# Kernel optimization log

Hardware: AMD Instinct MI355X
Metric: run time of the kernel (lower is better)

The kernel has to match this reference:

```python
import jax, jax.numpy as jnp
import numpy as np

B, S, D = 2, 2048, 1024
H = 16
HD = D // H  # head_dim = 64


def _xavier(key, shape):
    fan_out, fan_in = shape
    bound = jnp.sqrt(6.0 / (fan_in + fan_out))
    return jax.random.uniform(key, shape, jnp.float32, -bound, bound)


def setup_inputs() -> dict:
    key = jax.random.key(0)
    kx, kqkv, ko = jax.random.split(key, 3)
    x = jax.random.normal(kx, (B, S, D), jnp.float32)
    # torch nn.Linear stores weight as [out, in]; we keep that layout and use x @ W.T
    W_qkv = _xavier(kqkv, (3 * D, D))
    b_qkv = jnp.zeros((3 * D,), jnp.float32)
    W_o = _xavier(ko, (D, D))
    b_o = jnp.zeros((D,), jnp.float32)
    return {"x": x, "W_qkv": W_qkv, "b_qkv": b_qkv, "W_o": W_o, "b_o": b_o}


def reference(x, W_qkv, b_qkv, W_o, b_o):
    b, s, d = x.shape
    h, hd = H, HD
    # qkv projection: [b, s, 3d]
    qkv = jnp.einsum("bsd,ed->bse", x, W_qkv) + b_qkv
    # [b, s, h, 3*hd] -> [b, h, s, 3*hd]
    qkv = qkv.reshape(b, s, h, 3 * hd).transpose(0, 2, 1, 3)
    q, k, v = jnp.split(qkv, 3, axis=-1)
    scale = 1.0 / jnp.sqrt(jnp.asarray(hd, x.dtype))
    logits = jnp.einsum("bhqd,bhkd->bhqk", q, k) * scale
    attn = jax.nn.softmax(logits, axis=-1)
    values = jnp.einsum("bhqk,bhkd->bhqd", attn, v)
    values = values.transpose(0, 2, 1, 3).reshape(b, s, d)
    return jnp.einsum("bsd,ed->bse", values, W_o) + b_o
```

## Files before the change

### kernel.cpp

```cpp
#include <hip/hip_runtime.h>

typedef unsigned short u16;
typedef __attribute__((ext_vector_type(8))) short bf16x8;
typedef __attribute__((ext_vector_type(4))) float f32x4;
typedef __attribute__((ext_vector_type(16))) float f32x16;
typedef __attribute__((ext_vector_type(4))) unsigned short u16x4;

__device__ __forceinline__ u16 f2bf(float f) {
    unsigned u = __float_as_uint(f);
    u = u + 0x7FFFu + ((u >> 16) & 1u);
    return (u16)(u >> 16);
}

__device__ __forceinline__ void gload16(const void* g, void* l) {
    __builtin_amdgcn_global_load_lds(
        (const __attribute__((address_space(1))) unsigned int*)g,
        (__attribute__((address_space(3))) unsigned int*)l,
        16, 0, 0);
}

__device__ __forceinline__ f32x4 mfma16(bf16x8 a, bf16x8 b, f32x4 c) {
    return __builtin_amdgcn_mfma_f32_16x16x32_bf16(a, b, c, 0, 0, 0);
}
__device__ __forceinline__ f32x16 mfma32(bf16x8 a, bf16x8 b, f32x16 c) {
    return __builtin_amdgcn_mfma_f32_32x32x16_bf16(a, b, c, 0, 0, 0);
}

__global__ __launch_bounds__(256) void cvt_all(const float* __restrict__ x,
                                               const float* __restrict__ wqkv,
                                               const float* __restrict__ wo,
                                               u16* __restrict__ dst) {
    int i = blockIdx.x * 256 + threadIdx.x;
    float4 v;
    if (i < 1048576)       v = ((const float4*)x)[i];
    else if (i < 1835008)  v = ((const float4*)wqkv)[i - 1048576];
    else                   v = ((const float4*)wo)[i - 1835008];
    u16x4 o = { f2bf(v.x), f2bf(v.y), f2bf(v.z), f2bf(v.w) };
    ((u16x4*)dst)[i] = o;
}

template <int BM, int BN, bool OUT_BF16>
__global__ __launch_bounds__(256) void gemm_bt(const u16* __restrict__ A,
                                               const u16* __restrict__ Bm,
                                               const float* __restrict__ bias,
                                               void* __restrict__ Cp,
                                               int M, int N, int K) {
    constexpr int FM = BM / 32, FN = BN / 32;
    __shared__ u16 As[2][BM * 64];
    __shared__ u16 Bs[2][BN * 64];
    const int tid = threadIdx.x, lane = tid & 63, wave = tid >> 6;
    const int wr = wave >> 1, wc = wave & 1;
    const int l15 = lane & 15, l4 = lane >> 4;

    const int nx = gridDim.x, nwg = nx * gridDim.y;
    const int id = blockIdx.y * nx + blockIdx.x;
    const int wg = (id & 7) * (nwg >> 3) + (id >> 3);
    const int m0 = (wg / nx) * BM, n0 = (wg % nx) * BN;

    f32x4 zero = {0.f, 0.f, 0.f, 0.f};
    f32x4 acc[FM][FN];
#pragma unroll
    for (int m = 0; m < FM; ++m)
#pragma unroll
        for (int n = 0; n < FN; ++n) acc[m][n] = zero;

#define STAGE_BT(tt, buf) {                                                 \
    _Pragma("unroll")                                                       \
    for (int i = 0; i < BM / 32; ++i) {                                     \
        int c = i * 256 + tid;                                              \
        int r = c >> 3, kc = (c & 7) ^ (r & 7);                             \
        gload16(A + (size_t)(m0 + r) * K + (tt) * 64 + kc * 8,              \
                &As[buf][(i * 256 + wave * 64) * 8]);                       \
    }                                                                       \
    _Pragma("unroll")                                                       \
    for (int i = 0; i < BN / 32; ++i) {                                     \
        int c = i * 256 + tid;                                              \
        int r = c >> 3, kc = (c & 7) ^ (r & 7);                             \
        gload16(Bm + (size_t)(n0 + r) * K + (tt) * 64 + kc * 8,             \
                &Bs[buf][(i * 256 + wave * 64) * 8]);                       \
    } }

    const int nt = K >> 6;
    STAGE_BT(0, 0);
    for (int t = 0; t < nt; ++t) {
        asm volatile("s_waitcnt vmcnt(0)" ::: "memory");
        asm volatile("s_barrier" ::: "memory");
        if (t < nt - 1) { STAGE_BT(t + 1, (t + 1) & 1); }
        const char* Asb = (const char*)As[t & 1];
        const char* Bsb = (const char*)Bs[t & 1];
#pragma unroll
        for (int kk = 0; kk < 2; ++kk) {
            bf16x8 af[FM], bfr[FN];
#pragma unroll
            for (int m = 0; m < FM; ++m) {
                int row = wr * (BM / 2) + m * 16 + l15;
                int ch = (kk * 4 + l4) ^ (row & 7);
                af[m] = *(const bf16x8*)(Asb + row * 128 + ch * 16);
            }
#pragma unroll
            for (int n = 0; n < FN; ++n) {
                int row = wc * (BN / 2) + n * 16 + l15;
                int ch = (kk * 4 + l4) ^ (row & 7);
                bfr[n] = *(const bf16x8*)(Bsb + row * 128 + ch * 16);
            }
#pragma unroll
            for (int m = 0; m < FM; ++m)
#pragma unroll
                for (int n = 0; n < FN; ++n)
                    acc[m][n] = mfma16(af[m], bfr[n], acc[m][n]);
        }
    }
#undef STAGE_BT
    float bv[FN];
#pragma unroll
    for (int n = 0; n < FN; ++n) bv[n] = bias[n0 + wc * (BN / 2) + n * 16 + l15];
#pragma unroll
    for (int m = 0; m < FM; ++m) {
#pragma unroll
        for (int j = 0; j < 4; ++j) {
            size_t row = (size_t)(m0 + wr * (BM / 2) + m * 16 + l4 * 4 + j);
#pragma unroll
            for (int n = 0; n < FN; ++n) {
                int col = n0 + wc * (BN / 2) + n * 16 + l15;
                float v = acc[m][n][j] + bv[n];
                if (OUT_BF16)
                    ((u16*)Cp)[row * (size_t)N + col] = f2bf(v);
                else
                    ((float*)Cp)[row * (size_t)N + col] = v;
            }
        }
    }
}

__global__ __launch_bounds__(512) void gemm256(const u16* __restrict__ A,
                                               const u16* __restrict__ Bm,
                                               const float* __restrict__ bias,
                                               u16* __restrict__ Cp,
                                               u16* __restrict__ Vt,
                                               int M, int N, int K) {
    __shared__ __align__(16) char lds[131072];
    const int tid = threadIdx.x, lane = tid & 63, wave = tid >> 6;
    const int wr = wave >> 2, wc = wave & 3;
    const int l15 = lane & 15, l4 = lane >> 4;

    const int nx = gridDim.x, nwg = nx * gridDim.y;
    const int id = blockIdx.y * nx + blockIdx.x;
    const int wg = (id & 7) * (nwg >> 3) + (id >> 3);
    const int m0 = (wg / nx) * 256, n0 = (wg % nx) * 256;

    const u16* asrc[2][2];
    const u16* bsrc[2][2];
#pragma unroll
    for (int q = 0; q < 2; ++q)
#pragma unroll
        for (int r = 0; r < 2; ++r) {
            int c = r * 512 + tid;
            int lr = c >> 3;
            int kc = (c & 7) ^ (lr & 7);
            asrc[q][r] = A  + (size_t)(m0 + lr + (lr & 64) + q * 64) * K + kc * 8;
            bsrc[q][r] = Bm + (size_t)(n0 + lr + (lr & 96) + q * 32) * K + kc * 8;
        }
    const int sd0 = wave * 1024;
    const int sd1 = 8192 + wave * 1024;

    const int roA = (wr * 64 + l15) * 128;
    const int roB = (wc * 32 + l15) * 128;
    int ch16[2];
#pragma unroll
    for (int kk = 0; kk < 2; ++kk) ch16[kk] = ((kk * 4 + l4) ^ (l15 & 7)) * 16;

    f32x4 zero = {0.f, 0.f, 0.f, 0.f};
    f32x4 acc[2][2][4][2];
#pragma unroll
    for (int a = 0; a < 2; ++a)
#pragma unroll
        for (int b = 0; b < 2; ++b)
#pragma unroll
            for (int c = 0; c < 4; ++c)
#pragma unroll
                for (int d = 0; d < 2; ++d) acc[a][b][c][d] = zero;

#define STG_A(q, tt) { char* rb = lds + (((tt) & 1) * 32768) + (q) * 16384;          \
        gload16(asrc[q][0] + (size_t)(tt) * 64, rb + sd0);                            \
        gload16(asrc[q][1] + (size_t)(tt) * 64, rb + sd1); }
#define STG_B(q, tt) { char* rb = lds + 65536 + (((tt) & 1) * 32768) + (q) * 16384;  \
        gload16(bsrc[q][0] + (size_t)(tt) * 64, rb + sd0);                            \
        gload16(bsrc[q][1] + (size_t)(tt) * 64, rb + sd1); }
#define MFMA_PH(MH, NH) {                                                             \
        __builtin_amdgcn_s_setprio(1);                                                \
        _Pragma("unroll")                                                             \
        for (int fm = 0; fm < 4; ++fm)                                                \
            _Pragma("unroll")                                                         \
            for (int fn = 0; fn < 2; ++fn)                                            \
                _Pragma("unroll")                                                     \
                for (int kk = 0; kk < 2; ++kk)                                        \
                    acc[MH][NH][fm][fn] =                                             \
                        mfma16(af[fm][kk], bfr[NH][fn][kk], acc[MH][NH][fm][fn]);     \
        __builtin_amdgcn_s_setprio(0); }

    STG_A(0, 0); STG_B(0, 0); STG_A(1, 0); STG_B(1, 0);
    asm volatile("s_waitcnt vmcnt(4)" ::: "memory");
    asm volatile("s_barrier" ::: "memory");

    bf16x8 af[4][2], bfr[2][2][2];
    const int nt = K >> 6;
    for (int t = 0; t < nt; ++t) {
        const char* Ab = lds + (t & 1) * 32768;
        const char* Bb = lds + 65536 + (t & 1) * 32768;
#pragma unroll
        for (int fm = 0; fm < 4; ++fm)
#pragma unroll
            for (int kk = 0; kk < 2; ++kk)
                af[fm][kk] = *(const bf16x8*)(Ab + roA + fm * 2048 + ch16[kk]);
#pragma unroll
        for (int fn = 0; fn < 2; ++fn)
#pragma unroll
            for (int kk = 0; kk < 2; ++kk)
                bfr[0][fn][kk] = *(const bf16x8*)(Bb + roB + fn * 2048 + ch16[kk]);
        if (t < nt - 1) STG_A(0, t + 1);
        asm volatile("s_barrier" ::: "memory");
        MFMA_PH(0, 0);
        asm volatile("s_barrier" ::: "memory");
#pragma unroll
        for (int fn = 0; fn < 2; ++fn)
#pragma unroll
            for (int kk = 0; kk < 2; ++kk)
                bfr[1][fn][kk] = *(const bf16x8*)(Bb + 16384 + roB + fn * 2048 + ch16[kk]);
        if (t < nt - 1) STG_B(0, t + 1);
        asm volatile("s_barrier" ::: "memory");
        MFMA_PH(0, 1);
        if (t < nt - 1) asm volatile("s_waitcnt vmcnt(4)" ::: "memory");
        else            asm volatile("s_waitcnt vmcnt(0)" ::: "memory");
        asm volatile("s_barrier" ::: "memory");
#pragma unroll
        for (int fm = 0; fm < 4; ++fm)
#pragma unroll
            for (int kk = 0; kk < 2; ++kk)
                af[fm][kk] = *(const bf16x8*)(Ab + 16384 + roA + fm * 2048 + ch16[kk]);
        if (t < nt - 1) STG_A(1, t + 1);
        asm volatile("s_barrier" ::: "memory");
        MFMA_PH(1, 0);
        asm volatile("s_barrier" ::: "memory");
        if (t < nt - 1) STG_B(1, t + 1);
        asm volatile("s_barrier" ::: "memory");
        MFMA_PH(1, 1);
        if (t < nt - 1) asm volatile("s_waitcnt vmcnt(4)" ::: "memory");
        asm volatile("s_barrier" ::: "memory");
    }
#undef STG_A
#undef STG_B
#undef MFMA_PH

    float bv[2][2];
#pragma unroll
    for (int nh = 0; nh < 2; ++nh)
#pragma unroll
        for (int fn = 0; fn < 2; ++fn)
            bv[nh][fn] = bias[n0 + wc * 64 + nh * 32 + fn * 16 + l15];
#pragma unroll
    for (int mh = 0; mh < 2; ++mh)
#pragma unroll
        for (int fm = 0; fm < 4; ++fm)
#pragma unroll
            for (int j = 0; j < 4; ++j) {
                size_t row = (size_t)(m0 + wr * 128 + mh * 64 + fm * 16 + l4 * 4 + j);
#pragma unroll
                for (int nh = 0; nh < 2; ++nh)
#pragma unroll
                    for (int fn = 0; fn < 2; ++fn) {
                        int col = n0 + wc * 64 + nh * 32 + fn * 16 + l15;
                        Cp[row * (size_t)N + col] =
                            f2bf(acc[mh][nh][fm][fn][j] + bv[nh][fn]);
                    }
            }

    const int b_ = m0 >> 11, s0_ = m0 & 2047;
    const int hmin = (n0 + 63) / 192;
    const int nV = ((hmin + 1) * 192 + 128 < n0 + 256) ? 128 : 64;
#pragma unroll
    for (int nh = 0; nh < 2; ++nh)
#pragma unroll
        for (int fn = 0; fn < 2; ++fn) {
            int col = n0 + wc * 64 + nh * 32 + fn * 16 + l15;
            int hh = col / 192;
            int dd = col - hh * 192 - 128;
            if (dd >= 0) {
                int vl = (hh - hmin) * 64 + dd;
#pragma unroll
                for (int mh = 0; mh < 2; ++mh)
#pragma unroll
                    for (int fm = 0; fm < 4; ++fm) {
                        int r0 = wr * 128 + mh * 64 + fm * 16 + l4 * 4;
                        u16x4 w = { f2bf(acc[mh][nh][fm][fn][0] + bv[nh][fn]),
                                    f2bf(acc[mh][nh][fm][fn][1] + bv[nh][fn]),
                                    f2bf(acc[mh][nh][fm][fn][2] + bv[nh][fn]),
                                    f2bf(acc[mh][nh][fm][fn][3] + bv[nh][fn]) };
                        *(u16x4*)(lds + vl * 520 + r0 * 2) = w;
                    }
            }
        }
    __syncthreads();
    {
        size_t vt_base = ((size_t)(b_ * 16 + hmin) * 64) * 2048 + s0_;
        int nchunks = nV * 64;
        for (int c = tid; c < nchunks; c += 512) {
            int vl = c >> 6, sl = c & 63;
            u16x4 w = *(const u16x4*)(lds + vl * 520 + sl * 8);
            *(u16x4*)(Vt + (size_t)vl * 2048 + vt_base + sl * 4) = w;
        }
    }
}

__global__ __launch_bounds__(512, 4) void attn_kernel(const u16* __restrict__ qkv,
                                                      const u16* __restrict__ Vt,
                                                      u16* __restrict__ vals) {
    __shared__ __align__(16) char lds[65536];
    const int L = blockIdx.x;
    const int ord = L >> 3;
    const int hb = (L & 7) * 4 + (ord >> 4);
    const int qt = ord & 15;
    const int h = hb & 15, b = hb >> 4;
    const int st8 = (ord & 1) << 3;
    const int tid = threadIdx.x, lane = tid & 63, wave = tid >> 6;
    const int gtid = tid & 255, qsub = wave & 3, kvh = wave >> 2;
    const int l31 = lane & 31, hi = lane >> 5;
    const float S2E = 0.18033688f;

    const u16* qbase = qkv + (size_t)(b * 2048 + qt * 128 + qsub * 32 + l31) * 3072 + h * 192;
    bf16x8 Qf[4];
#pragma unroll
    for (int ks = 0; ks < 4; ++ks) {
        bf16x8 q = *(const bf16x8*)(qbase + ks * 16 + hi * 8);
#pragma unroll
        for (int j = 0; j < 8; ++j) {
            float f = __uint_as_float(((unsigned)(u16)q[j]) << 16) * S2E;
            q[j] = (short)f2bf(f);
        }
        Qf[ks] = q;
    }

    const u16* kpb[2];
    const u16* vpb[2];
    int dst[2];
#pragma unroll
    for (int i = 0; i < 2; ++i) {
        int c = i * 256 + gtid;
        int fi = c >> 6, dl = c & 63;
        int mm = fi >> 2, ks = fi & 3;
        int row = mm * 32 + (dl & 31);
        int col = ks * 16 + (dl >> 5) * 8;
        kpb[i] = qkv + (size_t)(b * 2048 + kvh * 1024 + row) * 3072 + h * 192 + 64 + col;
        vpb[i] = Vt + ((size_t)((b * 16 + h) * 64 + row)) * 2048 + kvh * 1024 + col;
        dst[i] = fi * 512;
    }
    u16* Kst = (u16*)lds + kvh * 8192;
    u16* Vst = (u16*)lds + 16384 + kvh * 8192;

    f32x16 accO[2];
#pragma unroll
    for (int md = 0; md < 2; ++md)
#pragma unroll
        for (int r = 0; r < 16; ++r) accO[md][r] = 0.f;
    float accLs = 0.f;

    const char* KsL = (const char*)Kst + lane * 16;
    const char* VsL = (const char*)Vst + lane * 16;

#pragma unroll
    for (int i = 0; i < 2; ++i) gload16(kpb[i] + (size_t)st8 * 196608, Kst + dst[i]);
#pragma unroll
    for (int i = 0; i < 2; ++i) gload16(vpb[i] + (size_t)st8 * 64, Vst + dst[i]);

    for (int t = 0; t < 16; ++t) {
        asm volatile("s_waitcnt vmcnt(0)" ::: "memory");
        asm volatile("s_barrier" ::: "memory");

        if (t < 15) {
            int phys = (t + 1 + st8) & 15;
            u16* kd = Kst + ((t + 1) & 1) * 4096;
            u16* vd = Vst + ((t + 1) & 1) * 4096;
#pragma unroll
            for (int i = 0; i < 2; ++i) gload16(kpb[i] + (size_t)phys * 196608, kd + dst[i]);
#pragma unroll
            for (int i = 0; i < 2; ++i) gload16(vpb[i] + (size_t)phys * 64, vd + dst[i]);
        }

        const char* Kb = KsL + (t & 1) * 8192;
        const char* Vb = VsL + (t & 1) * 8192;

        f32x16 sc[2];
        __builtin_amdgcn_s_setprio(1);
#pragma unroll
        for (int m = 0; m < 2; ++m) {
            f32x16 c;
#pragma unroll
            for (int r = 0; r < 16; ++r) c[r] = 0.f;
#pragma unroll
            for (int ks = 0; ks < 4; ++ks) {
                bf16x8 kf = *(const bf16x8*)(Kb + (m * 4 + ks) * 1024);
                c = mfma32(kf, Qf[ks], c);
            }
            sc[m] = c;
        }
        __builtin_amdgcn_s_setprio(0);

        bf16x8 Pf[4];
#pragma unroll
        for (int r = 0; r < 16; ++r)
            sc[0][r] = __builtin_amdgcn_exp2f(sc[0][r]);
        {
            float q0 = (sc[0][0] + sc[0][1]) + (sc[0][2] + sc[0][3]);
            float q1 = (sc[0][4] + sc[0][5]) + (sc[0][6] + sc[0][7]);
            float q2 = (sc[0][8] + sc[0][9]) + (sc[0][10] + sc[0][11]);
            float q3 = (sc[0][12] + sc[0][13]) + (sc[0][14] + sc[0][15]);
            accLs += (q0 + q1) + (q2 + q3);
        }
        {
            unsigned W0[4], W1[4];
#pragma unroll
            for (int g = 0; g < 4; ++g) {
                asm("v_cvt_pk_bf16_f32 %0, %1, %2"
                    : "=v"(W0[g]) : "v"(sc[0][4 * g + 0]), "v"(sc[0][4 * g + 1]));
                asm("v_cvt_pk_bf16_f32 %0, %1, %2"
                    : "=v"(W1[g]) : "v"(sc[0][4 * g + 2]), "v"(sc[0][4 * g + 3]));
            }
#pragma unroll
            for (int kpair = 0; kpair < 2; ++kpair) {
                unsigned xa = W0[2 * kpair], ya = W0[2 * kpair + 1];
                unsigned xb = W1[2 * kpair], yb = W1[2 * kpair + 1];
                asm volatile("v_permlane32_swap_b32 %0, %1" : "+v"(xa), "+v"(ya));
                asm volatile("v_permlane32_swap_b32 %0, %1" : "+v"(xb), "+v"(yb));
                union { unsigned w[4]; bf16x8 v; } u;
                u.w[0] = xa; u.w[1] = xb; u.w[2] = ya; u.w[3] = yb;
                Pf[kpair] = u.v;
            }
        }

        __builtin_amdgcn_s_setprio(1);
#pragma unroll
        for (int md = 0; md < 2; ++md) {
            f32x16 c = accO[md];
#pragma unroll
            for (int ks = 0; ks < 2; ++ks) {
                bf16x8 vf = *(const bf16x8*)(Vb + (md * 4 + ks) * 1024);
                c = mfma32(vf, Pf[ks], c);
            }
            accO[md] = c;
        }
        __builtin_amdgcn_s_setprio(0);

#pragma unroll
        for (int r = 0; r < 16; ++r)
            sc[1][r] = __builtin_amdgcn_exp2f(sc[1][r]);
        {
            float q0 = (sc[1][0] + sc[1][1]) + (sc[1][2] + sc[1][3]);
            float q1 = (sc[1][4] + sc[1][5]) + (sc[1][6] + sc[1][7]);
            float q2 = (sc[1][8] + sc[1][9]) + (sc[1][10] + sc[1][11]);
            float q3 = (sc[1][12] + sc[1][13]) + (sc[1][14] + sc[1][15]);
            accLs += (q0 + q1) + (q2 + q3);
        }
        {
            unsigned W0[4], W1[4];
#pragma unroll
            for (int g = 0; g < 4; ++g) {
                asm("v_cvt_pk_bf16_f32 %0, %1, %2"
                    : "=v"(W0[g]) : "v"(sc[1][4 * g + 0]), "v"(sc[1][4 * g + 1]));
                asm("v_cvt_pk_bf16_f32 %0, %1, %2"
                    : "=v"(W1[g]) : "v"(sc[1][4 * g + 2]), "v"(sc[1][4 * g + 3]));
            }
#pragma unroll
            for (int kpair = 0; kpair < 2; ++kpair) {
                unsigned xa = W0[2 * kpair], ya = W0[2 * kpair + 1];
                unsigned xb = W1[2 * kpair], yb = W1[2 * kpair + 1];
                asm volatile("v_permlane32_swap_b32 %0, %1" : "+v"(xa), "+v"(ya));
                asm volatile("v_permlane32_swap_b32 %0, %1" : "+v"(xb), "+v"(yb));
                union { unsigned w[4]; bf16x8 v; } u;
                u.w[0] = xa; u.w[1] = xb; u.w[2] = ya; u.w[3] = yb;
                Pf[2 + kpair] = u.v;
            }
        }

        __builtin_amdgcn_s_setprio(1);
#pragma unroll
        for (int md = 0; md < 2; ++md) {
            f32x16 c = accO[md];
#pragma unroll
            for (int ks = 2; ks < 4; ++ks) {
                bf16x8 vf = *(const bf16x8*)(Vb + (md * 4 + ks) * 1024);
                c = mfma32(vf, Pf[ks], c);
            }
            accO[md] = c;
        }
        __builtin_amdgcn_s_setprio(0);
    }

    float lt;
    {
        float xa = accLs, xb = accLs;
        asm volatile("v_permlane32_swap_b32 %0, %1" : "+v"(xa), "+v"(xb));
        lt = xa + xb;
    }

    float* MO = (float*)lds;
    float* ML = (float*)(lds + 32768);
    __syncthreads();
    if (kvh == 1) {
        int r = qsub * 64 + lane;
#pragma unroll
        for (int md = 0; md < 2; ++md)
#pragma unroll
            for (int g = 0; g < 4; ++g)
#pragma unroll
                for (int j = 0; j < 4; ++j)
                    MO[(md * 16 + 4 * g + j) * 256 + r] = accO[md][4 * g + j];
        ML[r] = lt;
    }
    __syncthreads();
    if (kvh == 0) {
        int r = qsub * 64 + lane;
        float inv = 1.f / (lt + ML[r]);
        size_t rowoff = (size_t)(b * 2048 + qt * 128 + qsub * 32 + l31) * 1024 + h * 64;
#pragma unroll
        for (int md = 0; md < 2; ++md)
#pragma unroll
            for (int g = 0; g < 4; ++g) {
                float w0 = MO[(md * 16 + 4 * g + 0) * 256 + r];
                float w1 = MO[(md * 16 + 4 * g + 1) * 256 + r];
                float w2 = MO[(md * 16 + 4 * g + 2) * 256 + r];
                float w3 = MO[(md * 16 + 4 * g + 3) * 256 + r];
                u16x4 o = { f2bf((accO[md][4 * g + 0] + w0) * inv),
                            f2bf((accO[md][4 * g + 1] + w1) * inv),
                            f2bf((accO[md][4 * g + 2] + w2) * inv),
                            f2bf((accO[md][4 * g + 3] + w3) * inv) };
                *(u16x4*)(vals + rowoff + md * 32 + 8 * g + 4 * hi) = o;
            }
    }
}

extern "C" void kernel_launch(void* const* d_in, const int* in_sizes, int n_in,
                              void* d_out, int out_size, void* d_ws, size_t ws_size,
                              hipStream_t stream) {
    const float* x    = (const float*)d_in[0];
    const float* Wqkv = (const float*)d_in[1];
    const float* bqkv = (const float*)d_in[2];
    const float* Wo   = (const float*)d_in[3];
    const float* bo   = (const float*)d_in[4];
    float* out = (float*)d_out;

    char* ws = (char*)d_ws;
    u16* x_bf    = (u16*)(ws);
    u16* Wqkv_bf = (u16*)(ws + 8388608);
    u16* Wo_bf   = (u16*)(ws + 14680064);
    u16* qkv_bf  = (u16*)(ws + 16777216);
    u16* Vt      = (u16*)(ws + 41943040);
    u16* vals    = (u16*)(ws + 50331648);

    cvt_all<<<8192, 256, 0, stream>>>(x, Wqkv, Wo, x_bf);

    gemm256<<<dim3(12, 16), 512, 0, stream>>>(x_bf, Wqkv_bf, bqkv, qkv_bf, Vt,
                                              4096, 3072, 1024);

    attn_kernel<<<512, 512, 0, stream>>>(qkv_bf, Vt, vals);

    gemm_bt<128, 64, false><<<dim3(16, 32), 256, 0, stream>>>(vals, Wo_bf, bo,
                                                              (void*)out, 4096, 1024, 1024);
}
```

Measured before the change: 111.4 us.

## Retile QKV GEMM to 256x192 tiles aligned with per-head QKV blocks

Changes the QKV projection GEMM tile from 256x256 to 256x192, so each workgroup covers exactly one head's q,k,v columns. The grid grows from 192 to 256 workgroups, which fills the GPU's compute units more evenly. The V-transpose epilogue becomes simpler because the V slice always sits at the third 64-column group. The B staging, LDS layout, MFMA phase schedule and wait counts are reworked to match, at the cost of lower arithmetic intensity per tile.

```diff
diff --git a/kernel.cpp b/kernel.cpp
--- a/kernel.cpp
+++ b/kernel.cpp
@@ -132,13 +132,13 @@
     }
 }
 
-__global__ __launch_bounds__(512) void gemm256(const u16* __restrict__ A,
+__global__ __launch_bounds__(512) void gemm192(const u16* __restrict__ A,
                                                const u16* __restrict__ Bm,
                                                const float* __restrict__ bias,
                                                u16* __restrict__ Cp,
                                                u16* __restrict__ Vt,
                                                int M, int N, int K) {
-    __shared__ __align__(16) char lds[131072];
+    __shared__ __align__(16) char lds[114688];
     const int tid = threadIdx.x, lane = tid & 63, wave = tid >> 6;
     const int wr = wave >> 2, wc = wave & 3;
     const int l15 = lane & 15, l4 = lane >> 4;
@@ -146,10 +146,9 @@
     const int nx = gridDim.x, nwg = nx * gridDim.y;
     const int id = blockIdx.y * nx + blockIdx.x;
     const int wg = (id & 7) * (nwg >> 3) + (id >> 3);
-    const int m0 = (wg / nx) * 256, n0 = (wg % nx) * 256;
+    const int m0 = (wg / nx) * 256, n0 = (wg % nx) * 192;
 
     const u16* asrc[2][2];
-    const u16* bsrc[2][2];
 #pragma unroll
     for (int q = 0; q < 2; ++q)
 #pragma unroll
@@ -157,78 +156,70 @@
             int c = r * 512 + tid;
             int lr = c >> 3;
             int kc = (c & 7) ^ (lr & 7);
-            asrc[q][r] = A  + (size_t)(m0 + lr + (lr & 64) + q * 64) * K + kc * 8;
-            bsrc[q][r] = Bm + (size_t)(n0 + lr + (lr & 96) + q * 32) * K + kc * 8;
-        }
+            asrc[q][r] = A + (size_t)(m0 + lr + (lr & 64) + q * 64) * K + kc * 8;
+        }
+    const u16* bsrc[3];
+    {
+        int lr2 = tid >> 3;
+        int kc = (tid & 7) ^ (lr2 & 7);
+#pragma unroll
+        for (int r3 = 0; r3 < 3; ++r3)
+            bsrc[r3] = Bm + (size_t)(n0 + r3 * 64 + lr2) * K + kc * 8;
+    }
     const int sd0 = wave * 1024;
     const int sd1 = 8192 + wave * 1024;
 
     const int roA = (wr * 64 + l15) * 128;
-    const int roB = (wc * 32 + l15) * 128;
+    const int roB = (wc * 16 + l15) * 128;
     int ch16[2];
 #pragma unroll
     for (int kk = 0; kk < 2; ++kk) ch16[kk] = ((kk * 4 + l4) ^ (l15 & 7)) * 16;
 
     f32x4 zero = {0.f, 0.f, 0.f, 0.f};
-    f32x4 acc[2][2][4][2];
+    f32x4 acc[2][3][4];
 #pragma unroll
     for (int a = 0; a < 2; ++a)
 #pragma unroll
-        for (int b = 0; b < 2; ++b)
-#pragma unroll
-            for (int c = 0; c < 4; ++c)
-#pragma unroll
-                for (int d = 0; d < 2; ++d) acc[a][b][c][d] = zero;
-
-#define STG_A(q, tt) { char* rb = lds + (((tt) & 1) * 32768) + (q) * 16384;          \
-        gload16(asrc[q][0] + (size_t)(tt) * 64, rb + sd0);                            \
+        for (int b = 0; b < 3; ++b)
+#pragma unroll
+            for (int c = 0; c < 4; ++c) acc[a][b][c] = zero;
+
+#define STG_A(q, tt) { char* rb = lds + (((tt) & 1) * 32768) + (q) * 16384;           \
+        gload16(asrc[q][0] + (size_t)(tt) * 64, rb + sd0);                             \
         gload16(asrc[q][1] + (size_t)(tt) * 64, rb + sd1); }
-#define STG_B(q, tt) { char* rb = lds + 65536 + (((tt) & 1) * 32768) + (q) * 16384;  \
-        gload16(bsrc[q][0] + (size_t)(tt) * 64, rb + sd0);                            \
-        gload16(bsrc[q][1] + (size_t)(tt) * 64, rb + sd1); }
-#define MFMA_PH(MH, NH) {                                                             \
-        __builtin_amdgcn_s_setprio(1);                                                \
-        _Pragma("unroll")                                                             \
-        for (int fm = 0; fm < 4; ++fm)                                                \
-            _Pragma("unroll")                                                         \
-            for (int fn = 0; fn < 2; ++fn)                                            \
-                _Pragma("unroll")                                                     \
-                for (int kk = 0; kk < 2; ++kk)                                        \
-                    acc[MH][NH][fm][fn] =                                             \
-                        mfma16(af[fm][kk], bfr[NH][fn][kk], acc[MH][NH][fm][fn]);     \
-        __builtin_amdgcn_s_setprio(0); }
-
-    STG_A(0, 0); STG_B(0, 0); STG_A(1, 0); STG_B(1, 0);
-    asm volatile("s_waitcnt vmcnt(4)" ::: "memory");
+#define STG_B(r3, tt) { char* rb = lds + 65536 + (((tt) & 1) * 24576) + (r3) * 8192;  \
+        gload16(bsrc[r3] + (size_t)(tt) * 64, rb + wave * 1024); }
+#define MFMA_G(MH, TH, AF) {                                                           \
+        _Pragma("unroll")                                                              \
+        for (int fm = 0; fm < 4; ++fm)                                                 \
+            _Pragma("unroll")                                                          \
+            for (int kk = 0; kk < 2; ++kk)                                             \
+                acc[MH][TH][fm] = mfma16(AF[fm][kk], bfr[TH][kk], acc[MH][TH][fm]); }
+
+    STG_A(0, 0); STG_B(0, 0); STG_B(1, 0); STG_A(1, 0); STG_B(2, 0);
+    asm volatile("s_waitcnt vmcnt(3)" ::: "memory");
     asm volatile("s_barrier" ::: "memory");
 
-    bf16x8 af[4][2], bfr[2][2][2];
+    bf16x8 af0[4][2], af1[4][2], bfr[3][2];
     const int nt = K >> 6;
     for (int t = 0; t < nt; ++t) {
         const char* Ab = lds + (t & 1) * 32768;
-        const char* Bb = lds + 65536 + (t & 1) * 32768;
+        const char* Bb = lds + 65536 + (t & 1) * 24576;
 #pragma unroll
         for (int fm = 0; fm < 4; ++fm)
 #pragma unroll
             for (int kk = 0; kk < 2; ++kk)
-                af[fm][kk] = *(const bf16x8*)(Ab + roA + fm * 2048 + ch16[kk]);
-#pragma unroll
-        for (int fn = 0; fn < 2; ++fn)
+                af0[fm][kk] = *(const bf16x8*)(Ab + roA + fm * 2048 + ch16[kk]);
+#pragma unroll
+        for (int th = 0; th < 2; ++th)
 #pragma unroll
             for (int kk = 0; kk < 2; ++kk)
-                bfr[0][fn][kk] = *(const bf16x8*)(Bb + roB + fn * 2048 + ch16[kk]);
-        if (t < nt - 1) STG_A(0, t + 1);
-        asm volatile("s_barrier" ::: "memory");
-        MFMA_PH(0, 0);
-        asm volatile("s_barrier" ::: "memory");
-#pragma unroll
-        for (int fn = 0; fn < 2; ++fn)
-#pragma unroll
-            for (int kk = 0; kk < 2; ++kk)
-                bfr[1][fn][kk] = *(const bf16x8*)(Bb + 16384 + roB + fn * 2048 + ch16[kk]);
-        if (t < nt - 1) STG_B(0, t + 1);
-        asm volatile("s_barrier" ::: "memory");
-        MFMA_PH(0, 1);
+                bfr[th][kk] = *(const bf16x8*)(Bb + th * 8192 + roB + ch16[kk]);
+        if (t < nt - 1) { STG_A(0, t + 1); STG_B(0, t + 1); STG_B(1, t + 1); }
+        asm volatile("s_barrier" ::: "memory");
+        __builtin_amdgcn_s_setprio(1);
+        MFMA_G(0, 0, af0); MFMA_G(0, 1, af0);
+        __builtin_amdgcn_s_setprio(0);
         if (t < nt - 1) asm volatile("s_waitcnt vmcnt(4)" ::: "memory");
         else            asm volatile("s_waitcnt vmcnt(0)" ::: "memory");
         asm volatile("s_barrier" ::: "memory");
@@ -236,27 +227,31 @@
         for (int fm = 0; fm < 4; ++fm)
 #pragma unroll
             for (int kk = 0; kk < 2; ++kk)
-                af[fm][kk] = *(const bf16x8*)(Ab + 16384 + roA + fm * 2048 + ch16[kk]);
-        if (t < nt - 1) STG_A(1, t + 1);
-        asm volatile("s_barrier" ::: "memory");
-        MFMA_PH(1, 0);
-        asm volatile("s_barrier" ::: "memory");
-        if (t < nt - 1) STG_B(1, t + 1);
-        asm volatile("s_barrier" ::: "memory");
-        MFMA_PH(1, 1);
-        if (t < nt - 1) asm volatile("s_waitcnt vmcnt(4)" ::: "memory");
+                af1[fm][kk] = *(const bf16x8*)(Ab + 16384 + roA + fm * 2048 + ch16[kk]);
+#pragma unroll
+        for (int kk = 0; kk < 2; ++kk)
+            bfr[2][kk] = *(const bf16x8*)(Bb + 2 * 8192 + roB + ch16[kk]);
+        if (t < nt - 1) { STG_A(1, t + 1); }
+        asm volatile("s_barrier" ::: "memory");
+        __builtin_amdgcn_s_setprio(1);
+        MFMA_G(0, 2, af0); MFMA_G(1, 0, af1);
+        __builtin_amdgcn_s_setprio(0);
+        asm volatile("s_barrier" ::: "memory");
+        if (t < nt - 1) { STG_B(2, t + 1); }
+        asm volatile("s_barrier" ::: "memory");
+        __builtin_amdgcn_s_setprio(1);
+        MFMA_G(1, 1, af1); MFMA_G(1, 2, af1);
+        __builtin_amdgcn_s_setprio(0);
+        if (t < nt - 1) asm volatile("s_waitcnt vmcnt(3)" ::: "memory");
         asm volatile("s_barrier" ::: "memory");
     }
 #undef STG_A
 #undef STG_B
-#undef MFMA_PH
-
-    float bv[2][2];
-#pragma unroll
-    for (int nh = 0; nh < 2; ++nh)
-#pragma unroll
-        for (int fn = 0; fn < 2; ++fn)
-            bv[nh][fn] = bias[n0 + wc * 64 + nh * 32 + fn * 16 + l15];
+#undef MFMA_G
+
+    float bv[3];
+#pragma unroll
+    for (int th = 0; th < 3; ++th) bv[th] = bias[n0 + th * 64 + wc * 16 + l15];
 #pragma unroll
     for (int mh = 0; mh < 2; ++mh)
 #pragma unroll
@@ -265,48 +260,33 @@
             for (int j = 0; j < 4; ++j) {
                 size_t row = (size_t)(m0 + wr * 128 + mh * 64 + fm * 16 + l4 * 4 + j);
 #pragma unroll
-                for (int nh = 0; nh < 2; ++nh)
-#pragma unroll
-                    for (int fn = 0; fn < 2; ++fn) {
-                        int col = n0 + wc * 64 + nh * 32 + fn * 16 + l15;
-                        Cp[row * (size_t)N + col] =
-                            f2bf(acc[mh][nh][fm][fn][j] + bv[nh][fn]);
-                    }
+                for (int th = 0; th < 3; ++th) {
+                    int col = n0 + th * 64 + wc * 16 + l15;
+                    Cp[row * (size_t)N + col] = f2bf(acc[mh][th][fm][j] + bv[th]);
+                }
             }
 
     const int b_ = m0 >> 11, s0_ = m0 & 2047;
-    const int hmin = (n0 + 63) / 192;
-    const int nV = ((hmin + 1) * 192 + 128 < n0 + 256) ? 128 : 64;
-#pragma unroll
-    for (int nh = 0; nh < 2; ++nh)
-#pragma unroll
-        for (int fn = 0; fn < 2; ++fn) {
-            int col = n0 + wc * 64 + nh * 32 + fn * 16 + l15;
-            int hh = col / 192;
-            int dd = col - hh * 192 - 128;
-            if (dd >= 0) {
-                int vl = (hh - hmin) * 64 + dd;
-#pragma unroll
-                for (int mh = 0; mh < 2; ++mh)
-#pragma unroll
-                    for (int fm = 0; fm < 4; ++fm) {
-                        int r0 = wr * 128 + mh * 64 + fm * 16 + l4 * 4;
-                        u16x4 w = { f2bf(acc[mh][nh][fm][fn][0] + bv[nh][fn]),
-                                    f2bf(acc[mh][nh][fm][fn][1] + bv[nh][fn]),
-                                    f2bf(acc[mh][nh][fm][fn][2] + bv[nh][fn]),
-                                    f2bf(acc[mh][nh][fm][fn][3] + bv[nh][fn]) };
-                        *(u16x4*)(lds + vl * 520 + r0 * 2) = w;
-                    }
-            }
+    const int h = n0 / 192;
+    const int vl = wc * 16 + l15;
+#pragma unroll
+    for (int mh = 0; mh < 2; ++mh)
+#pragma unroll
+        for (int fm = 0; fm < 4; ++fm) {
+            int r0 = wr * 128 + mh * 64 + fm * 16 + l4 * 4;
+            u16x4 w = { f2bf(acc[mh][2][fm][0] + bv[2]),
+                        f2bf(acc[mh][2][fm][1] + bv[2]),
+                        f2bf(acc[mh][2][fm][2] + bv[2]),
+                        f2bf(acc[mh][2][fm][3] + bv[2]) };
+            *(u16x4*)(lds + vl * 520 + r0 * 2) = w;
         }
     __syncthreads();
     {
-        size_t vt_base = ((size_t)(b_ * 16 + hmin) * 64) * 2048 + s0_;
-        int nchunks = nV * 64;
-        for (int c = tid; c < nchunks; c += 512) {
-            int vl = c >> 6, sl = c & 63;
-            u16x4 w = *(const u16x4*)(lds + vl * 520 + sl * 8);
-            *(u16x4*)(Vt + (size_t)vl * 2048 + vt_base + sl * 4) = w;
+        size_t vt_base = ((size_t)(b_ * 16 + h) * 64) * 2048 + s0_;
+        for (int c = tid; c < 4096; c += 512) {
+            int vl2 = c >> 6, sl = c & 63;
+            u16x4 w = *(const u16x4*)(lds + vl2 * 520 + sl * 8);
+            *(u16x4*)(Vt + (size_t)vl2 * 2048 + vt_base + sl * 4) = w;
         }
     }
 }
@@ -557,7 +537,7 @@
 
     cvt_all<<<8192, 256, 0, stream>>>(x, Wqkv, Wo, x_bf);
 
-    gemm256<<<dim3(12, 16), 512, 0, stream>>>(x_bf, Wqkv_bf, bqkv, qkv_bf, Vt,
+    gemm192<<<dim3(16, 16), 512, 0, stream>>>(x_bf, Wqkv_bf, bqkv, qkv_bf, Vt,
                                               4096, 3072, 1024);
 
     attn_kernel<<<512, 512, 0, stream>>>(qkv_bf, Vt, vals);
```

Result: faster. 105.8 us (-5.0%).
